# Kernel optimization log

Measured on AMD Instinct MI355X. Metric: run time of the kernel, lower is better.

The kernel has to match this reference:

```python
import jax, jax.numpy as jnp
import numpy as np
from jax import lax

C_IN, C_OUT, K, N_BASE, HIDDEN = 256, 256, 3, 8, 128
ATT_TAU = 1.0


def setup_inputs() -> dict:
    key = jax.random.key(0)
    ks = jax.random.split(key, 6)
    B, H, W = 64, 64, 64
    x = jax.random.normal(ks[0], (B, C_IN, H, W), dtype=jnp.float32)
    # attention MLP params (torch Linear convention: W is [out, in])
    w1 = jax.random.normal(ks[1], (HIDDEN, C_IN), dtype=jnp.float32) * (1.0 / np.sqrt(C_IN))
    b1 = jnp.zeros((HIDDEN,), dtype=jnp.float32)
    w2 = jax.random.normal(ks[2], (C_OUT * N_BASE, HIDDEN), dtype=jnp.float32) * (1.0 / np.sqrt(HIDDEN))
    b2 = jnp.zeros((C_OUT * N_BASE,), dtype=jnp.float32)
    # base filters: kaiming-normal over flat [n_base, c_in*k*k]
    fan_in = C_IN * K * K
    base_filters = jax.random.normal(ks[3], (N_BASE, fan_in), dtype=jnp.float32) * np.sqrt(2.0 / fan_in)
    return {"x": x, "w1": w1, "b1": b1, "w2": w2, "b2": b2, "base_filters": base_filters}


def reference(x, w1, b1, w2, b2, base_filters):
    B = x.shape[0]
    # global average pool -> [B, c_in]
    pooled = x.mean(axis=(2, 3))
    # attention MLP -> per-sample mixing weights [B, c_out, n_base]
    h = jax.nn.relu(pooled @ w1.T + b1)
    mix = (h @ w2.T + b2).reshape(B, C_OUT, N_BASE)
    mix = jax.nn.softmax(mix / ATT_TAU, axis=2)
    # base conv: [B, c_in, H, W] -> [B, n_base, H, W], SAME padding (k//2)
    filt = base_filters.reshape(N_BASE, C_IN, K, K)
    pad = K // 2
    y = lax.conv_general_dilated(
        x, filt, window_strides=(1, 1), padding=[(pad, pad), (pad, pad)],
        dimension_numbers=("NCHW", "OIHW", "NCHW"))
    # per-sample 1x1 mixing conv == batched matmul over channels
    out = jnp.einsum("bon,bnhw->bohw", mix, y)
    return out
```

## Files before the change

### kernel.cpp

```cpp
#include <hip/hip_runtime.h>
#include <math.h>

#define CIN 256
#define COUT 256
#define NB 8
#define HID 128
#define HW 4096
#define BATCH 64

#define TROWS 18
#define XS 64

typedef float f32x4 __attribute__((ext_vector_type(4)));

__global__ __launch_bounds__(256) void repack_filters(
    const float* __restrict__ bf, float* __restrict__ fT) {
  int i = blockIdx.x * 256 + threadIdx.x;
  if (i < 8 * 2304) {
    int n = i / 2304;
    int cd = i % 2304;
    fT[cd * 8 + n] = bf[i];
  }
}

__global__ __launch_bounds__(256, 4) void conv_pool_kernel(
    const float* __restrict__ x, const float* __restrict__ fT,
    float* __restrict__ ypart, float* __restrict__ poolpart) {
  __shared__ float xs[8 * TROWS * XS];
  const int t = threadIdx.x;
  const int bid = blockIdx.x;
  const int b = bid >> 4;
  const int g = (bid >> 2) & 3;
  const int rc = bid & 3;
  const int row0 = rc * 16;
  const int c0 = g * 64;

  const int ch = t >> 5;
  const int part = t & 31;
  const int p16 = part >> 4;
  const int seg = part & 15;
  const int r = t >> 4;
  const int cg = t & 15;

  float4 v[9];
  {
    const float* xsrc0 = x + ((size_t)(b * CIN + c0 + ch) * HW);
#pragma unroll
    for (int i = 0; i < 9; ++i) {
      const int grow = row0 - 1 + 2 * i + p16;
      if ((unsigned)grow < 64u)
        v[i] = *(const float4*)(xsrc0 + grow * 64 + seg * 4);
    }
  }
  __builtin_amdgcn_sched_barrier(0);

  {
    float4 z4 = {0.0f, 0.0f, 0.0f, 0.0f};
    for (int i = t; i < 8 * TROWS * XS / 4; i += 256)
      *(float4*)&xs[i * 4] = z4;
  }

  float acc[8][4];
#pragma unroll
  for (int n = 0; n < 8; ++n)
#pragma unroll
    for (int j = 0; j < 4; ++j) acc[n][j] = 0.0f;

#pragma unroll 1
  for (int chunk = 0; chunk < 8; ++chunk) {
    const int cbase = c0 + chunk * 8;

    __syncthreads();

    float psum = 0.0f;
#pragma unroll
    for (int i = 0; i < 9; ++i) {
      const int row = 2 * i + p16;
      const int grow = row0 - 1 + row;
      if ((unsigned)grow < 64u) {
        *(float4*)&xs[(ch * TROWS + row) * XS + seg * 4] = v[i];
        if (row >= 1 && row <= 16)
          psum += (v[i].x + v[i].y) + (v[i].z + v[i].w);
      }
    }
#pragma unroll
    for (int off = 16; off > 0; off >>= 1)
      psum += __shfl_down(psum, off, 32);
    if (part == 0)
      poolpart[(b * 4 + rc) * 256 + cbase + ch] = psum;
    __syncthreads();

    if (chunk < 7) {
      const float* xsrc = x + ((size_t)(b * CIN + cbase + 8 + ch) * HW);
#pragma unroll
      for (int i = 0; i < 9; ++i) {
        const int grow = row0 - 1 + 2 * i + p16;
        if ((unsigned)grow < 64u)
          v[i] = *(const float4*)(xsrc + grow * 64 + seg * 4);
      }
    }
    __builtin_amdgcn_sched_barrier(0);

#pragma unroll
    for (int cc = 0; cc < 8; ++cc) {
      const float* fb = fT + (size_t)(cbase + cc) * 72;
      const float* xrow = &xs[(cc * TROWS + r) * XS + cg * 4];
#pragma unroll
      for (int dy = 0; dy < 3; ++dy) {
        float4 a0 = *(const float4*)(xrow + dy * XS);
        float wl = __shfl_up(a0.w, 1, 16);
        float wr = __shfl_down(a0.x, 1, 16);
        float w[6];
        w[0] = (cg == 0) ? 0.0f : wl;
        w[1] = a0.x; w[2] = a0.y; w[3] = a0.z; w[4] = a0.w;
        w[5] = (cg == 15) ? 0.0f : wr;
#pragma unroll
        for (int dx = 0; dx < 3; ++dx) {
#pragma unroll
          for (int n = 0; n < 8; ++n) {
            const float fv = fb[(dy * 3 + dx) * 8 + n];
#pragma unroll
            for (int j = 0; j < 4; ++j)
              acc[n][j] = fmaf(w[j + dx], fv, acc[n][j]);
          }
        }
      }
    }
  }

#pragma unroll
  for (int n = 0; n < 8; ++n) {
    float* yp = ypart +
        ((size_t)(((b * 4 + g) * 8 + n) * 64 + row0 + r) * 64 + cg * 4);
    float4 v0 = {acc[n][0], acc[n][1], acc[n][2], acc[n][3]};
    *(float4*)(yp) = v0;
  }
}

__global__ __launch_bounds__(256) void mlp_kernel(
    const float* __restrict__ poolpart, const float* __restrict__ w1,
    const float* __restrict__ b1, const float* __restrict__ w2,
    const float* __restrict__ b2, float* __restrict__ mix) {
  __shared__ float pool_s[256];
  __shared__ float h_s[128];
  const int t = threadIdx.x;
  const int b = blockIdx.x;
  pool_s[t] = (poolpart[(b * 4 + 0) * 256 + t] +
               poolpart[(b * 4 + 1) * 256 + t] +
               poolpart[(b * 4 + 2) * 256 + t] +
               poolpart[(b * 4 + 3) * 256 + t]) * (1.0f / 4096.0f);
  __syncthreads();
  if (t < 128) {
    float a = b1[t];
    const float* wr = w1 + t * 256;
    for (int c = 0; c < 256; c += 4) {
      float4 wv = *(const float4*)(wr + c);
      a = fmaf(pool_s[c], wv.x, a);
      a = fmaf(pool_s[c + 1], wv.y, a);
      a = fmaf(pool_s[c + 2], wv.z, a);
      a = fmaf(pool_s[c + 3], wv.w, a);
    }
    h_s[t] = fmaxf(a, 0.0f);
  }
  __syncthreads();
  float m[8];
#pragma unroll
  for (int n = 0; n < 8; ++n) {
    float a = b2[t * 8 + n];
    const float* wr = w2 + (size_t)(t * 8 + n) * 128;
    for (int j = 0; j < 128; j += 4) {
      float4 wv = *(const float4*)(wr + j);
      a = fmaf(h_s[j], wv.x, a);
      a = fmaf(h_s[j + 1], wv.y, a);
      a = fmaf(h_s[j + 2], wv.z, a);
      a = fmaf(h_s[j + 3], wv.w, a);
    }
    m[n] = a;
  }
  float mx = m[0];
#pragma unroll
  for (int n = 1; n < 8; ++n) mx = fmaxf(mx, m[n]);
  float s = 0.0f;
#pragma unroll
  for (int n = 0; n < 8; ++n) {
    m[n] = __expf(m[n] - mx);
    s += m[n];
  }
  float inv = 1.0f / s;
#pragma unroll
  for (int n = 0; n < 8; ++n) mix[(size_t)(b * 256 + t) * 8 + n] = m[n] * inv;
}

__global__ __launch_bounds__(256, 4) void mix_conv_kernel(
    const float* __restrict__ ypart, const float* __restrict__ mix,
    float* __restrict__ out) {
  __shared__ float ys[8 * 1024];
  const int t = threadIdx.x;
  const int bid = blockIdx.x;
  const int b = bid >> 3;
  const int tile = (bid >> 1) & 3;
  const int oh = bid & 1;
  const int p0 = tile * 1024;

  const float* yb = ypart + (size_t)b * 4 * 8 * HW + p0;
  for (int i = t; i < 2048; i += 256) {
    int n = i >> 8;
    int pv = i & 255;
    const float* y0 = yb + n * HW + pv * 4;
    float4 a = *(const float4*)(y0);
    float4 c = *(const float4*)(y0 + 8 * HW);
    float4 d = *(const float4*)(y0 + 16 * HW);
    float4 e = *(const float4*)(y0 + 24 * HW);
    float4 rr = {a.x + c.x + d.x + e.x, a.y + c.y + d.y + e.y,
                 a.z + c.z + d.z + e.z, a.w + c.w + d.w + e.w};
    *(float4*)&ys[n * 1024 + pv * 4] = rr;
  }
  __syncthreads();

  float4 y4[8];
#pragma unroll
  for (int n = 0; n < 8; ++n) y4[n] = *(const float4*)&ys[n * 1024 + t * 4];

  const float* mixb = mix + ((size_t)b * 256 + oh * 128) * 8;
  float* op = out + ((size_t)b * COUT + oh * 128) * HW + p0 + t * 4;
#pragma unroll 2
  for (int o = 0; o < 128; ++o) {
    const float* mp = mixb + o * 8;
    float4 ma = *(const float4*)(mp);
    float4 mb = *(const float4*)(mp + 4);
    float4 r;
    r.x = ma.x * y4[0].x; r.y = ma.x * y4[0].y;
    r.z = ma.x * y4[0].z; r.w = ma.x * y4[0].w;
    r.x = fmaf(ma.y, y4[1].x, r.x); r.y = fmaf(ma.y, y4[1].y, r.y);
    r.z = fmaf(ma.y, y4[1].z, r.z); r.w = fmaf(ma.y, y4[1].w, r.w);
    r.x = fmaf(ma.z, y4[2].x, r.x); r.y = fmaf(ma.z, y4[2].y, r.y);
    r.z = fmaf(ma.z, y4[2].z, r.z); r.w = fmaf(ma.z, y4[2].w, r.w);
    r.x = fmaf(ma.w, y4[3].x, r.x); r.y = fmaf(ma.w, y4[3].y, r.y);
    r.z = fmaf(ma.w, y4[3].z, r.z); r.w = fmaf(ma.w, y4[3].w, r.w);
    r.x = fmaf(mb.x, y4[4].x, r.x); r.y = fmaf(mb.x, y4[4].y, r.y);
    r.z = fmaf(mb.x, y4[4].z, r.z); r.w = fmaf(mb.x, y4[4].w, r.w);
    r.x = fmaf(mb.y, y4[5].x, r.x); r.y = fmaf(mb.y, y4[5].y, r.y);
    r.z = fmaf(mb.y, y4[5].z, r.z); r.w = fmaf(mb.y, y4[5].w, r.w);
    r.x = fmaf(mb.z, y4[6].x, r.x); r.y = fmaf(mb.z, y4[6].y, r.y);
    r.z = fmaf(mb.z, y4[6].z, r.z); r.w = fmaf(mb.z, y4[6].w, r.w);
    r.x = fmaf(mb.w, y4[7].x, r.x); r.y = fmaf(mb.w, y4[7].y, r.y);
    r.z = fmaf(mb.w, y4[7].z, r.z); r.w = fmaf(mb.w, y4[7].w, r.w);
    f32x4 rn = {r.x, r.y, r.z, r.w};
    __builtin_nontemporal_store(rn, (f32x4*)(op + (size_t)o * HW));
  }
}

extern "C" void kernel_launch(void* const* d_in, const int* in_sizes, int n_in,
                              void* d_out, int out_size, void* d_ws,
                              size_t ws_size, hipStream_t stream) {
  const float* x  = (const float*)d_in[0];
  const float* w1 = (const float*)d_in[1];
  const float* b1 = (const float*)d_in[2];
  const float* w2 = (const float*)d_in[3];
  const float* b2 = (const float*)d_in[4];
  const float* bf = (const float*)d_in[5];
  float* out = (float*)d_out;

  char* ws = (char*)d_ws;
  float* ypart    = (float*)(ws);
  float* poolpart = (float*)(ws + 33554432);
  float* mixw     = (float*)(ws + 33554432 + 262144);
  float* fT       = (float*)(ws + 33554432 + 262144 + 2097152);

  repack_filters<<<72, 256, 0, stream>>>(bf, fT);
  conv_pool_kernel<<<1024, 256, 0, stream>>>(x, fT, ypart, poolpart);
  mlp_kernel<<<64, 256, 0, stream>>>(poolpart, w1, b1, w2, b2, mixw);
  mix_conv_kernel<<<512, 256, 0, stream>>>(ypart, mixw, out);
}
```

Measured before the change: 646.8 us.

## Double-buffer conv input tiles via direct global-to-LDS async loads

Replaces the register-staged prefetch of input rows with __builtin_amdgcn_global_load_lds writes straight into a second LDS buffer, so the next channel chunk loads while the current one is computed. Synchronisation now uses manual s_waitcnt vmcnt and s_barrier instead of __syncthreads, and pooling sums are read back from LDS. This frees the 36 VGPRs that held staged data and removes the register-to-LDS store pass. In exchange it doubles LDS use and drops the occupancy hint from launch_bounds, which may lower occupancy. The vmcnt(9) count assumes all nine loads are issued, but boundary rows skip their loads, so the wait may be inexact at edges.

```diff
diff --git a/kernel.cpp b/kernel.cpp
--- a/kernel.cpp
+++ b/kernel.cpp
@@ -10,6 +10,7 @@
 
 #define TROWS 18
 #define XS 64
+#define BUFN (8 * TROWS * XS)
 
 typedef float f32x4 __attribute__((ext_vector_type(4)));
 
@@ -23,10 +24,10 @@
   }
 }
 
-__global__ __launch_bounds__(256, 4) void conv_pool_kernel(
+__global__ __launch_bounds__(256) void conv_pool_kernel(
     const float* __restrict__ x, const float* __restrict__ fT,
     float* __restrict__ ypart, float* __restrict__ poolpart) {
-  __shared__ float xs[8 * TROWS * XS];
+  __shared__ float xs[2][BUFN];
   const int t = threadIdx.x;
   const int bid = blockIdx.x;
   const int b = bid >> 4;
@@ -35,6 +36,8 @@
   const int row0 = rc * 16;
   const int c0 = g * 64;
 
+  const int w = t >> 6;
+  const int l = t & 63;
   const int ch = t >> 5;
   const int part = t & 31;
   const int p16 = part >> 4;
@@ -42,23 +45,35 @@
   const int r = t >> 4;
   const int cg = t & 15;
 
-  float4 v[9];
   {
-    const float* xsrc0 = x + ((size_t)(b * CIN + c0 + ch) * HW);
-#pragma unroll
-    for (int i = 0; i < 9; ++i) {
-      const int grow = row0 - 1 + 2 * i + p16;
-      if ((unsigned)grow < 64u)
-        v[i] = *(const float4*)(xsrc0 + grow * 64 + seg * 4);
-    }
-  }
-  __builtin_amdgcn_sched_barrier(0);
-
-  {
+    float* xsf = &xs[0][0];
     float4 z4 = {0.0f, 0.0f, 0.0f, 0.0f};
-    for (int i = t; i < 8 * TROWS * XS / 4; i += 256)
-      *(float4*)&xs[i * 4] = z4;
-  }
+    for (int i = t; i < 2 * BUFN / 4; i += 256) *(float4*)&xsf[i * 4] = z4;
+  }
+  __syncthreads();
+
+#define STAGE(bufsel, cb)                                                    \
+  {                                                                          \
+    _Pragma("unroll") for (int i = 0; i < 9; ++i) {                          \
+      const int il = i * 64 + l;                                             \
+      const int c1 = (il >= 288) ? 1 : 0;     \
+      const int chs = 2 * w + c1;                                            \
+      const int rem = il - 288 * c1;                                         \
+      const int rows_ = rem >> 4;                                            \
+      const int segs_ = rem & 15;                                            \
+      const int grow_ = row0 - 1 + rows_;                                    \
+      if ((unsigned)grow_ < 64u)    \
+        __builtin_amdgcn_global_load_lds(                                    \
+            (__attribute__((address_space(1))) unsigned int*)(               \
+                x + ((size_t)(b * CIN + (cb) + chs) * HW + grow_ * 64 +      \
+                     segs_ * 4)),                                            \
+            (__attribute__((address_space(3))) unsigned int*)(               \
+                &xs[bufsel][(w * 9 + i) * 256]),                             \
+            16, 0, 0);                                                       \
+    }                                                                        \
+  }
+
+  STAGE(0, c0);
 
   float acc[8][4];
 #pragma unroll
@@ -68,19 +83,24 @@
 
 #pragma unroll 1
   for (int chunk = 0; chunk < 8; ++chunk) {
+    const int cur = chunk & 1;
     const int cbase = c0 + chunk * 8;
 
-    __syncthreads();
+    if (chunk < 7) {
+      STAGE(cur ^ 1, cbase + 8);
+      asm volatile("s_waitcnt vmcnt(9)" ::: "memory");
+    } else {
+      asm volatile("s_waitcnt vmcnt(0)" ::: "memory");
+    }
+    asm volatile("s_barrier" ::: "memory");
 
     float psum = 0.0f;
 #pragma unroll
     for (int i = 0; i < 9; ++i) {
       const int row = 2 * i + p16;
-      const int grow = row0 - 1 + row;
-      if ((unsigned)grow < 64u) {
-        *(float4*)&xs[(ch * TROWS + row) * XS + seg * 4] = v[i];
-        if (row >= 1 && row <= 16)
-          psum += (v[i].x + v[i].y) + (v[i].z + v[i].w);
+      if (row >= 1 && row <= 16) {
+        float4 pv = *(const float4*)&xs[cur][(ch * TROWS + row) * XS + seg * 4];
+        psum += (pv.x + pv.y) + (pv.z + pv.w);
       }
     }
 #pragma unroll
@@ -88,32 +108,20 @@
       psum += __shfl_down(psum, off, 32);
     if (part == 0)
       poolpart[(b * 4 + rc) * 256 + cbase + ch] = psum;
-    __syncthreads();
-
-    if (chunk < 7) {
-      const float* xsrc = x + ((size_t)(b * CIN + cbase + 8 + ch) * HW);
-#pragma unroll
-      for (int i = 0; i < 9; ++i) {
-        const int grow = row0 - 1 + 2 * i + p16;
-        if ((unsigned)grow < 64u)
-          v[i] = *(const float4*)(xsrc + grow * 64 + seg * 4);
-      }
-    }
-    __builtin_amdgcn_sched_barrier(0);
 
 #pragma unroll
     for (int cc = 0; cc < 8; ++cc) {
       const float* fb = fT + (size_t)(cbase + cc) * 72;
-      const float* xrow = &xs[(cc * TROWS + r) * XS + cg * 4];
+      const float* xrow = &xs[cur][(cc * TROWS + r) * XS + cg * 4];
 #pragma unroll
       for (int dy = 0; dy < 3; ++dy) {
         float4 a0 = *(const float4*)(xrow + dy * XS);
         float wl = __shfl_up(a0.w, 1, 16);
         float wr = __shfl_down(a0.x, 1, 16);
-        float w[6];
-        w[0] = (cg == 0) ? 0.0f : wl;
-        w[1] = a0.x; w[2] = a0.y; w[3] = a0.z; w[4] = a0.w;
-        w[5] = (cg == 15) ? 0.0f : wr;
+        float w6[6];
+        w6[0] = (cg == 0) ? 0.0f : wl;
+        w6[1] = a0.x; w6[2] = a0.y; w6[3] = a0.z; w6[4] = a0.w;
+        w6[5] = (cg == 15) ? 0.0f : wr;
 #pragma unroll
         for (int dx = 0; dx < 3; ++dx) {
 #pragma unroll
@@ -121,12 +129,16 @@
             const float fv = fb[(dy * 3 + dx) * 8 + n];
 #pragma unroll
             for (int j = 0; j < 4; ++j)
-              acc[n][j] = fmaf(w[j + dx], fv, acc[n][j]);
+              acc[n][j] = fmaf(w6[j + dx], fv, acc[n][j]);
           }
         }
       }
     }
-  }
+
+    asm volatile("s_waitcnt lgkmcnt(0)" ::: "memory");
+    asm volatile("s_barrier" ::: "memory");
+  }
+#undef STAGE
 
 #pragma unroll
   for (int n = 0; n < 8; ++n) {
```

Result: faster. 600.0 us (-7.2%).
